# Optimization experiments

Hardware: AMD Instinct MI355X
Metric: run time of the kernel (lower is better)

The kernel has to match this reference:

```python
import jax, jax.numpy as jnp
import numpy as np

N = 4096        # nodes
E = 131072      # edges (avg degree 32)
IN = 256        # in_channels
OUT = 64        # out_channels per head
HEADS = 4


def setup_inputs() -> dict:
    key = jax.random.key(0)
    k1, k2, k3, k4 = jax.random.split(key, 4)
    h = jax.random.normal(k1, (N, IN), dtype=jnp.float32)
    edge_index = jax.random.randint(k2, (2, E), 0, N, dtype=jnp.int64)
    # Linear weights, one per head: [HEADS, OUT, IN] (torch Linear layout)
    W = jax.random.normal(k3, (HEADS, OUT, IN), dtype=jnp.float32) * (1.0 / np.sqrt(IN))
    # attention vector a: xavier_uniform with gain=1.414, shape [2*OUT, 1]
    limit = 1.414 * np.sqrt(6.0 / (2 * OUT + 1))
    a = jax.random.uniform(k4, (HEADS, 2 * OUT, 1), dtype=jnp.float32, minval=-limit, maxval=limit)
    return {"h": h, "edge_index": edge_index, "W": W, "a": a}


def _head(h, row, col, Wf, af):
    # Wh = Linear(h): [N, OUT]
    Wh = h @ Wf.T
    # e = leakyrelu(cat(Wh[row], Wh[col]) @ a) == Wh[row]@a1 + Wh[col]@a2
    a1 = af[:OUT, 0]
    a2 = af[OUT:, 0]
    e = jax.nn.leaky_relu(Wh[row] @ a1 + Wh[col] @ a2, negative_slope=0.2)
    # dense N x N scatter (faithful to original: non-edges contribute exp(0))
    alpha = jnp.zeros((h.shape[0], h.shape[0]), dtype=h.dtype).at[row, col].set(e)
    alpha = jax.nn.softmax(alpha, axis=1)
    h_prime = alpha @ Wh  # [N, OUT]
    return h_prime, alpha


def reference(h, edge_index, W, a):
    row, col = edge_index[0], edge_index[1]
    # vmap over heads: h_prime [HEADS, N, OUT], attn [HEADS, N, N]
    h_prime, attn = jax.vmap(lambda Wf, af: _head(h, row, col, Wf, af))(W, a)
    # concat heads along features, then relu
    out = jax.nn.relu(jnp.transpose(h_prime, (1, 0, 2)).reshape(h.shape[0], HEADS * OUT))
    return out, attn.mean(axis=0)
```

## Files before the change

kernel.cpp:

```cpp
#include <hip/hip_runtime.h>

#define N_NODES 4096
#define E_EDGES 131072
#define IN_F    256
#define OUT_F   64
#define HEADS   4
#define HC      256
#define CAP     128

#define PREP_BLOCKS ((N_NODES * IN_F + HC * IN_F) / 256)
#define APP_BLOCKS  (E_EDGES / 256)

typedef float v4f __attribute__((ext_vector_type(4)));
typedef short v8s __attribute__((ext_vector_type(8)));
typedef float v4acc __attribute__((ext_vector_type(4)));

__device__ __forceinline__ unsigned short bf16_rn(float x) {
    unsigned u = __builtin_bit_cast(unsigned, x);
    unsigned r = (u + 0x7FFFu + ((u >> 16) & 1u)) >> 16;
    return (unsigned short)r;
}
__device__ __forceinline__ float bf16_to_f(unsigned short b) {
    unsigned u = ((unsigned)b) << 16;
    return __builtin_bit_cast(float, u);
}

__global__ void k_prep_append(const float* __restrict__ h, const float* __restrict__ W,
                              unsigned short* __restrict__ h_hi, unsigned short* __restrict__ h_lo,
                              unsigned short* __restrict__ W_hi, unsigned short* __restrict__ W_lo,
                              const int* __restrict__ rows,
                              int* __restrict__ rowcnt, int* __restrict__ slots) {
    const int b = blockIdx.x;
    if (b < PREP_BLOCKS) {
        const int i = b * 256 + threadIdx.x;
        const int HN = N_NODES * IN_F;
        if (i < HN) {
            float x = h[i];
            unsigned short hi = bf16_rn(x);
            h_hi[i] = hi;
            h_lo[i] = bf16_rn(x - bf16_to_f(hi));
        } else {
            int j = i - HN;
            float x = W[j];
            unsigned short hi = bf16_rn(x);
            W_hi[j] = hi;
            W_lo[j] = bf16_rn(x - bf16_to_f(hi));
        }
    } else {
        const int k = (b - PREP_BLOCKS) * 256 + threadIdx.x;
        const int r = rows[k];
        const int pos = atomicAdd(&rowcnt[r], 1);
        if (pos < CAP) slots[r * CAP + pos] = k;
    }
}

__global__ __launch_bounds__(256) void k_linear_mfma(
        const unsigned short* __restrict__ h_hi, const unsigned short* __restrict__ h_lo,
        const unsigned short* __restrict__ W_hi, const unsigned short* __restrict__ W_lo,
        const float* __restrict__ a,
        float* __restrict__ Wh, float* __restrict__ s1, float* __restrict__ s2,
        float* __restrict__ S) {
    const int t = threadIdx.x;
    const int wave = t >> 6, lane = t & 63;
    const int n16 = lane & 15, quad = lane >> 4;
    const int node0 = blockIdx.x * 16;
    const int ch0 = wave * 64;
    const int head = wave;

    v4acc acc[4];
#pragma unroll
    for (int nt = 0; nt < 4; ++nt) acc[nt] = (v4acc){0.f, 0.f, 0.f, 0.f};

    const int arow = (node0 + n16) * IN_F;
#pragma unroll
    for (int s = 0; s < 8; ++s) {
        const int k0 = s * 32 + quad * 8;
        v8s Ah = *(const v8s*)(h_hi + arow + k0);
        v8s Al = *(const v8s*)(h_lo + arow + k0);
#pragma unroll
        for (int nt = 0; nt < 4; ++nt) {
            const int ch = ch0 + nt * 16 + n16;
            v8s Bh = *(const v8s*)(W_hi + ch * IN_F + k0);
            v8s Bl = *(const v8s*)(W_lo + ch * IN_F + k0);
            acc[nt] = __builtin_amdgcn_mfma_f32_16x16x32_bf16(Ah, Bh, acc[nt], 0, 0, 0);
            acc[nt] = __builtin_amdgcn_mfma_f32_16x16x32_bf16(Ah, Bl, acc[nt], 0, 0, 0);
            acc[nt] = __builtin_amdgcn_mfma_f32_16x16x32_bf16(Al, Bh, acc[nt], 0, 0, 0);
        }
    }

#pragma unroll
    for (int nt = 0; nt < 4; ++nt) {
        const int ch = ch0 + nt * 16 + n16;
#pragma unroll
        for (int r = 0; r < 4; ++r)
            Wh[(size_t)(node0 + quad * 4 + r) * HC + ch] = acc[nt][r];
    }

    float a1v[4], a2v[4];
#pragma unroll
    for (int nt = 0; nt < 4; ++nt) {
        a1v[nt] = a[head * 2 * OUT_F + nt * 16 + n16];
        a2v[nt] = a[head * 2 * OUT_F + OUT_F + nt * 16 + n16];
    }
#pragma unroll
    for (int r = 0; r < 4; ++r) {
        float p1 = acc[0][r] * a1v[0] + acc[1][r] * a1v[1] + acc[2][r] * a1v[2] + acc[3][r] * a1v[3];
        float p2 = acc[0][r] * a2v[0] + acc[1][r] * a2v[1] + acc[2][r] * a2v[2] + acc[3][r] * a2v[3];
#pragma unroll
        for (int o = 1; o < 16; o <<= 1) {
            p1 += __shfl_xor(p1, o, 64);
            p2 += __shfl_xor(p2, o, 64);
        }
        if (n16 == 0) {
            const int node = node0 + quad * 4 + r;
            s1[node * HEADS + head] = p1;
            s2[node * HEADS + head] = p2;
        }
    }

#pragma unroll
    for (int nt = 0; nt < 4; ++nt) {
        float cp = acc[nt][0] + acc[nt][1] + acc[nt][2] + acc[nt][3];
        cp += __shfl_xor(cp, 16, 64);
        cp += __shfl_xor(cp, 32, 64);
        if (quad == 0) atomicAdd(&S[ch0 + nt * 16 + n16], cp);
    }
}

__global__ __launch_bounds__(256) void k_stats(
        const int* __restrict__ rowcnt, const int* __restrict__ slots,
        const int* __restrict__ cols,
        const float* __restrict__ s1, const float* __restrict__ s2,
        const float* __restrict__ S, const float* __restrict__ Wh,
        float* __restrict__ out0, float* __restrict__ bsum,
        int* __restrict__ gnw, int* __restrict__ gcol, float* __restrict__ gws) {
    __shared__ float eh[HEADS][CAP];
    __shared__ int   kk[CAP];
    __shared__ int   cc[CAP];
    __shared__ int   wcol[CAP];
    __shared__ float weh[HEADS][CAP];
    __shared__ float wgt[HEADS][CAP];
    __shared__ float mh[HEADS], dh[HEADS], bh[HEADS];
    __shared__ int   nw_sh;

    const int i = blockIdx.x;
    const int t = threadIdx.x, head = t >> 6, lane = t & 63;
    int cnt = rowcnt[i];
    if (cnt > CAP) cnt = CAP;
    if (t == 0) nw_sh = 0;

    const float4 s1r = *(const float4*)(s1 + i * HEADS);

    for (int q = t; q < cnt; q += 256) {
        const int k = slots[i * CAP + q];
        const int c = cols[k];
        kk[q] = k; cc[q] = c;
        const float4 s2c = *(const float4*)(s2 + c * HEADS);
        float x;
        x = s1r.x + s2c.x; eh[0][q] = (x > 0.f) ? x : 0.2f * x;
        x = s1r.y + s2c.y; eh[1][q] = (x > 0.f) ? x : 0.2f * x;
        x = s1r.z + s2c.z; eh[2][q] = (x > 0.f) ? x : 0.2f * x;
        x = s1r.w + s2c.w; eh[3][q] = (x > 0.f) ? x : 0.2f * x;
    }
    __syncthreads();

    for (int q = t; q < cnt; q += 256) {
        const int c = cc[q], k = kk[q];
        int win = 1;
        for (int q2 = 0; q2 < cnt; ++q2)
            if (cc[q2] == c && kk[q2] > k) { win = 0; break; }
        if (win) {
            const int pos = atomicAdd(&nw_sh, 1);
            wcol[pos] = c;
            weh[0][pos] = eh[0][q]; weh[1][pos] = eh[1][q];
            weh[2][pos] = eh[2][q]; weh[3][pos] = eh[3][q];
        }
    }
    __syncthreads();
    const int nw = nw_sh;

    float emax = -1e30f;
    for (int q = lane; q < nw; q += 64) emax = fmaxf(emax, weh[head][q]);
#pragma unroll
    for (int o = 32; o > 0; o >>= 1) emax = fmaxf(emax, __shfl_xor(emax, o, 64));
    const float m = fmaxf(emax, 0.f);

    float ssum = 0.f;
    for (int q = lane; q < nw; q += 64) ssum += __expf(weh[head][q] - m);
#pragma unroll
    for (int o = 32; o > 0; o >>= 1) ssum += __shfl_xor(ssum, o, 64);

    if (lane == 0) {
        const float denom = ssum + (float)(N_NODES - nw) * __expf(-m);
        mh[head] = m;
        dh[head] = denom;
        bh[head] = __expf(-m) / denom;
    }
    __syncthreads();

    for (int q = t; q < nw; q += 256) {
        const float w0 = __expf(weh[0][q] - mh[0]) / dh[0];
        const float w1 = __expf(weh[1][q] - mh[1]) / dh[1];
        const float w2 = __expf(weh[2][q] - mh[2]) / dh[2];
        const float w3 = __expf(weh[3][q] - mh[3]) / dh[3];
        wgt[0][q] = w0; wgt[1][q] = w1; wgt[2][q] = w2; wgt[3][q] = w3;
        gcol[i * CAP + q] = wcol[q];
        gws[i * CAP + q]  = 0.25f * (w0 + w1 + w2 + w3);
    }
    if (t == 0) {
        gnw[i] = nw;
        bsum[i] = 0.25f * (bh[0] + bh[1] + bh[2] + bh[3]);
    }
    __syncthreads();

    const float b_ = bh[head];
    float acc = b_ * S[t];
    for (int q = 0; q < nw; ++q)
        acc += (wgt[head][q] - b_) * Wh[(size_t)wcol[q] * HC + t];
    out0[(size_t)i * HC + t] = fmaxf(acc, 0.f);
}

__global__ __launch_bounds__(256) void k_attn(
        const float* __restrict__ bsum, const int* __restrict__ gnw,
        const int* __restrict__ gcol, const float* __restrict__ gws,
        float* __restrict__ attn) {
    __shared__ float rowbuf[N_NODES];
    const int i = blockIdx.x, t = threadIdx.x;
    const float v = bsum[i];
    const int nw = gnw[i];
    const float4 v4 = make_float4(v, v, v, v);
    float4* rb4 = (float4*)rowbuf;
#pragma unroll
    for (int rep = 0; rep < 4; ++rep) rb4[rep * 256 + t] = v4;
    __syncthreads();
    for (int q = t; q < nw; q += 256) rowbuf[gcol[i * CAP + q]] = gws[i * CAP + q];
    __syncthreads();
    const float4* src = (const float4*)rowbuf;
    float4* dst = (float4*)(attn + (size_t)i * N_NODES);
#pragma unroll
    for (int rep = 0; rep < 4; ++rep)
        dst[rep * 256 + t] = src[rep * 256 + t];
}

extern "C" void kernel_launch(void* const* d_in, const int* in_sizes, int n_in,
                              void* d_out, int out_size, void* d_ws, size_t ws_size,
                              hipStream_t stream) {
    const float* h  = (const float*)d_in[0];
    const int*   ei = (const int*)d_in[1];
    const float* W  = (const float*)d_in[2];
    const float* a  = (const float*)d_in[3];
    const int* rows = ei;
    const int* cols = ei + E_EDGES;

    float* out0 = (float*)d_out;
    float* attn = out0 + (size_t)N_NODES * HC;

    char* p = (char*)d_ws;
    auto carve = [&](size_t bytes) { char* q = p; p += (bytes + 255) & ~(size_t)255; return q; };
    float* S       = (float*)carve(sizeof(float) * HC + sizeof(int) * N_NODES);
    int*   rowcnt  = (int*)(S + HC);
    float* Wh      = (float*)carve(sizeof(float) * (size_t)N_NODES * HC);
    float* s1      = (float*)carve(sizeof(float) * N_NODES * HEADS);
    float* s2      = (float*)carve(sizeof(float) * N_NODES * HEADS);
    float* bsum    = (float*)carve(sizeof(float) * N_NODES);
    int*   slots   = (int*)carve(sizeof(int) * (size_t)N_NODES * CAP);
    int*   gnw     = (int*)carve(sizeof(int) * N_NODES);
    int*   gcol    = (int*)carve(sizeof(int) * (size_t)N_NODES * CAP);
    float* gws     = (float*)carve(sizeof(float) * (size_t)N_NODES * CAP);
    unsigned short* h_hi = (unsigned short*)carve(sizeof(short) * (size_t)N_NODES * IN_F);
    unsigned short* h_lo = (unsigned short*)carve(sizeof(short) * (size_t)N_NODES * IN_F);
    unsigned short* W_hi = (unsigned short*)carve(sizeof(short) * HC * IN_F);
    unsigned short* W_lo = (unsigned short*)carve(sizeof(short) * HC * IN_F);

    hipMemsetAsync(S, 0, sizeof(float) * HC + sizeof(int) * N_NODES, stream);
    k_prep_append<<<PREP_BLOCKS + APP_BLOCKS, 256, 0, stream>>>(
        h, W, h_hi, h_lo, W_hi, W_lo, rows, rowcnt, slots);
    k_linear_mfma<<<N_NODES / 16, 256, 0, stream>>>(h_hi, h_lo, W_hi, W_lo, a, Wh, s1, s2, S);
    k_stats<<<N_NODES, 256, 0, stream>>>(rowcnt, slots, cols, s1, s2, S, Wh,
                                         out0, bsum, gnw, gcol, gws);
    k_attn<<<N_NODES, 256, 0, stream>>>(bsum, gnw, gcol, gws, attn);
}
```

Measured before the change: 148.9 us.

## Fold memset into prep, move edge bucketing into linear kernel, vectorize and nontemporal stores

Removes the hipMemsetAsync by zeroing rowcnt and S inside the prep kernel, and vectorizes the bf16 hi/lo split to float4 loads and ushort4 stores. Edge bucketing by row moves from the prep kernel into the MFMA linear kernel, which runs 256 blocks each handling 512 edges. Output and attention-matrix stores use nontemporal hints so the large attention write does not pollute cache. Each change saves a launch or some memory traffic. In exchange, the MFMA kernel now waits on atomics before it starts its matmul work.

```diff
diff --git a/kernel.cpp b/kernel.cpp
--- a/kernel.cpp
+++ b/kernel.cpp
@@ -8,9 +8,6 @@
 #define HC      256
 #define CAP     128
 
-#define PREP_BLOCKS ((N_NODES * IN_F + HC * IN_F) / 256)
-#define APP_BLOCKS  (E_EDGES / 256)
-
 typedef float v4f __attribute__((ext_vector_type(4)));
 typedef short v8s __attribute__((ext_vector_type(8)));
 typedef float v4acc __attribute__((ext_vector_type(4)));
@@ -25,42 +22,50 @@
     return __builtin_bit_cast(float, u);
 }
 
-__global__ void k_prep_append(const float* __restrict__ h, const float* __restrict__ W,
-                              unsigned short* __restrict__ h_hi, unsigned short* __restrict__ h_lo,
-                              unsigned short* __restrict__ W_hi, unsigned short* __restrict__ W_lo,
-                              const int* __restrict__ rows,
-                              int* __restrict__ rowcnt, int* __restrict__ slots) {
-    const int b = blockIdx.x;
-    if (b < PREP_BLOCKS) {
-        const int i = b * 256 + threadIdx.x;
-        const int HN = N_NODES * IN_F;
-        if (i < HN) {
-            float x = h[i];
-            unsigned short hi = bf16_rn(x);
-            h_hi[i] = hi;
-            h_lo[i] = bf16_rn(x - bf16_to_f(hi));
-        } else {
-            int j = i - HN;
-            float x = W[j];
-            unsigned short hi = bf16_rn(x);
-            W_hi[j] = hi;
-            W_lo[j] = bf16_rn(x - bf16_to_f(hi));
-        }
-    } else {
-        const int k = (b - PREP_BLOCKS) * 256 + threadIdx.x;
-        const int r = rows[k];
-        const int pos = atomicAdd(&rowcnt[r], 1);
-        if (pos < CAP) slots[r * CAP + pos] = k;
-    }
+__global__ __launch_bounds__(256) void k_prep(
+        const float* __restrict__ h, const float* __restrict__ W,
+        unsigned short* __restrict__ h_hi, unsigned short* __restrict__ h_lo,
+        unsigned short* __restrict__ W_hi, unsigned short* __restrict__ W_lo,
+        int* __restrict__ rowcnt, float* __restrict__ S) {
+    const int tid = blockIdx.x * 256 + threadIdx.x;
+    if (tid < N_NODES) rowcnt[tid] = 0;
+    else if (tid < N_NODES + HC) S[tid - N_NODES] = 0.f;
+
+    const int HN4 = (N_NODES * IN_F) / 4;
+    const float4* src;
+    unsigned short *dhi, *dlo;
+    int j;
+    if (tid < HN4) { src = (const float4*)h; dhi = h_hi; dlo = h_lo; j = tid; }
+    else           { src = (const float4*)W; dhi = W_hi; dlo = W_lo; j = tid - HN4; }
+    const float4 x = src[j];
+    const unsigned short hx = bf16_rn(x.x), hy = bf16_rn(x.y), hz = bf16_rn(x.z), hw = bf16_rn(x.w);
+    ushort4 hi4 = make_ushort4(hx, hy, hz, hw);
+    ushort4 lo4 = make_ushort4(bf16_rn(x.x - bf16_to_f(hx)), bf16_rn(x.y - bf16_to_f(hy)),
+                               bf16_rn(x.z - bf16_to_f(hz)), bf16_rn(x.w - bf16_to_f(hw)));
+    *(ushort4*)(dhi + j * 4) = hi4;
+    *(ushort4*)(dlo + j * 4) = lo4;
 }
 
 __global__ __launch_bounds__(256) void k_linear_mfma(
         const unsigned short* __restrict__ h_hi, const unsigned short* __restrict__ h_lo,
         const unsigned short* __restrict__ W_hi, const unsigned short* __restrict__ W_lo,
-        const float* __restrict__ a,
+        const float* __restrict__ a, const int* __restrict__ rows,
+        int* __restrict__ rowcnt, int* __restrict__ slots,
         float* __restrict__ Wh, float* __restrict__ s1, float* __restrict__ s2,
         float* __restrict__ S) {
     const int t = threadIdx.x;
+
+    {
+        const int e0 = blockIdx.x * 512 + t;
+#pragma unroll
+        for (int rep = 0; rep < 2; ++rep) {
+            const int k = e0 + rep * 256;
+            const int r = rows[k];
+            const int pos = atomicAdd(&rowcnt[r], 1);
+            if (pos < CAP) slots[r * CAP + pos] = k;
+        }
+    }
+
     const int wave = t >> 6, lane = t & 63;
     const int n16 = lane & 15, quad = lane >> 4;
     const int node0 = blockIdx.x * 16;
@@ -217,7 +222,7 @@
     float acc = b_ * S[t];
     for (int q = 0; q < nw; ++q)
         acc += (wgt[head][q] - b_) * Wh[(size_t)wcol[q] * HC + t];
-    out0[(size_t)i * HC + t] = fmaxf(acc, 0.f);
+    __builtin_nontemporal_store(fmaxf(acc, 0.f), out0 + (size_t)i * HC + t);
 }
 
 __global__ __launch_bounds__(256) void k_attn(
@@ -235,11 +240,11 @@
     __syncthreads();
     for (int q = t; q < nw; q += 256) rowbuf[gcol[i * CAP + q]] = gws[i * CAP + q];
     __syncthreads();
-    const float4* src = (const float4*)rowbuf;
-    float4* dst = (float4*)(attn + (size_t)i * N_NODES);
+    const v4f* src = (const v4f*)rowbuf;
+    v4f* dst = (v4f*)(attn + (size_t)i * N_NODES);
 #pragma unroll
     for (int rep = 0; rep < 4; ++rep)
-        dst[rep * 256 + t] = src[rep * 256 + t];
+        __builtin_nontemporal_store(src[rep * 256 + t], &dst[rep * 256 + t]);
 }
 
 extern "C" void kernel_launch(void* const* d_in, const int* in_sizes, int n_in,
@@ -257,8 +262,8 @@
 
     char* p = (char*)d_ws;
     auto carve = [&](size_t bytes) { char* q = p; p += (bytes + 255) & ~(size_t)255; return q; };
-    float* S       = (float*)carve(sizeof(float) * HC + sizeof(int) * N_NODES);
-    int*   rowcnt  = (int*)(S + HC);
+    float* S       = (float*)carve(sizeof(float) * HC);
+    int*   rowcnt  = (int*)carve(sizeof(int) * N_NODES);
     float* Wh      = (float*)carve(sizeof(float) * (size_t)N_NODES * HC);
     float* s1      = (float*)carve(sizeof(float) * N_NODES * HEADS);
     float* s2      = (float*)carve(sizeof(float) * N_NODES * HEADS);
@@ -272,10 +277,10 @@
     unsigned short* W_hi = (unsigned short*)carve(sizeof(short) * HC * IN_F);
     unsigned short* W_lo = (unsigned short*)carve(sizeof(short) * HC * IN_F);
 
-    hipMemsetAsync(S, 0, sizeof(float) * HC + sizeof(int) * N_NODES, stream);
-    k_prep_append<<<PREP_BLOCKS + APP_BLOCKS, 256, 0, stream>>>(
-        h, W, h_hi, h_lo, W_hi, W_lo, rows, rowcnt, slots);
-    k_linear_mfma<<<N_NODES / 16, 256, 0, stream>>>(h_hi, h_lo, W_hi, W_lo, a, Wh, s1, s2, S);
+    k_prep<<<(N_NODES * IN_F + HC * IN_F) / 4 / 256, 256, 0, stream>>>(
+        h, W, h_hi, h_lo, W_hi, W_lo, rowcnt, S);
+    k_linear_mfma<<<N_NODES / 16, 256, 0, stream>>>(h_hi, h_lo, W_hi, W_lo, a, rows,
+                                                    rowcnt, slots, Wh, s1, s2, S);
     k_stats<<<N_NODES, 256, 0, stream>>>(rowcnt, slots, cols, s1, s2, S, Wh,
                                          out0, bsum, gnw, gcol, gws);
     k_attn<<<N_NODES, 256, 0, stream>>>(bsum, gnw, gcol, gws, attn);
```

New measurement: 143.4 us, median of 2. 3.7% less time.
